# Optimization experiments

Measured on AMD Instinct MI355X. Metric: run time of the kernel, lower is better.

The kernel has to match this reference:

```python
import jax, jax.numpy as jnp
import numpy as np

N_STATES = 256
N_FEATURES = 32000
SEQ_LEN = 8192


def setup_inputs() -> dict:
    key = jax.random.key(0)
    k1, k2, k3, k4 = jax.random.split(key, 4)
    startprob = jax.random.uniform(k1, (N_STATES,), dtype=jnp.float32)
    startprob = startprob / startprob.sum()
    transmat = jax.random.uniform(k2, (N_STATES, N_STATES), dtype=jnp.float32)
    transmat = transmat / transmat.sum(axis=1, keepdims=True)
    emissionprob = jax.random.uniform(k3, (N_STATES, N_FEATURES), dtype=jnp.float32)
    emissionprob = emissionprob / emissionprob.sum(axis=1, keepdims=True)
    obs = jax.random.randint(k4, (SEQ_LEN,), 0, N_FEATURES, dtype=jnp.int64)
    return {"startprob": startprob, "transmat": transmat,
            "emissionprob": emissionprob, "obs": obs}


def reference(startprob, transmat, emissionprob, obs):
    """HMM forward algorithm (order-1, log-space).

    Returns alpha of shape (n_states, T) where
    alpha[i, t] = log P(O_1..O_t, q_t = S_i | theta).
    """
    log_start = jnp.log(startprob)                # [N]
    log_A = jnp.log(transmat)                     # [N, N]
    log_E = jnp.log(emissionprob)                 # [N, V]
    log_e_obs = log_E[:, obs].T                   # [T, N] gathered emissions

    alpha0 = log_start + log_e_obs[0]             # [N]

    def step(prev, log_e_t):
        # logsumexp over source state i: prev[i] + log_A[i, j]
        a = jax.nn.logsumexp(prev[:, None] + log_A, axis=0) + log_e_t
        return a, a

    _, alphas = jax.lax.scan(step, alpha0, log_e_obs[1:])   # [T-1, N]
    alpha = jnp.concatenate([alpha0[None, :], alphas], axis=0)  # [T, N]
    return alpha.T                                 # [N, T]
```

## Files before the change

kernel.cpp:

```cpp
#include <hip/hip_runtime.h>
#include <hip/hip_bf16.h>
#include <math.h>

#define NS 256
#define T_LEN 8192
#define NF 32000
#define L_CH 2
#define B_BN 8
#define S_TOT 10
#define C_CH 4096
#define G_CH 16
#define NBLK 256
#define SCALE 32768.0f
#define XPAD 264
#define TCHUNK 512

typedef short short8 __attribute__((ext_vector_type(8)));
typedef float f32x4 __attribute__((ext_vector_type(4)));

__device__ __forceinline__ short f2bs(float f) {
    union { __bf16 b; short s; } u; u.b = (__bf16)f; return u.s;
}
__device__ __forceinline__ float bs2f(short s) {
    union { short s; __bf16 b; } u; u.s = s; return (float)u.b;
}

__device__ __forceinline__ void sync_lds_only() {
    __builtin_amdgcn_sched_barrier(0);
    asm volatile("s_waitcnt lgkmcnt(0)" ::: "memory");
    __builtin_amdgcn_s_barrier();
    __builtin_amdgcn_sched_barrier(0);
}

__global__ __launch_bounds__(256)
void prep(const float* __restrict__ E, const int* __restrict__ obs,
          const float* __restrict__ A,
          unsigned short* __restrict__ SEb, short* __restrict__ Aswz) {
    const int bid = blockIdx.x;
    if (bid < 256) {
        const int jg = bid & 15, tc = bid >> 4;
        const int t0 = tc * TCHUNK;
        __shared__ int olds[TCHUNK];
        for (int i = threadIdx.x; i < TCHUNK; i += 256)
            olds[i] = obs[t0 + i];
        __syncthreads();
        const int jl = threadIdx.x & 15;
        const int tl = threadIdx.x >> 4;
        const int j  = jg * 16 + jl;
        const float* Erow = E + (size_t)j * NF;
#pragma unroll 4
        for (int p = 0; p < TCHUNK / 16; ++p) {
            int t_loc = p * 16 + tl;
            int o = olds[t_loc];
            SEb[(size_t)(t0 + t_loc) * NS + j] =
                (unsigned short)f2bs(Erow[o] * SCALE);
        }
    } else if (bid < 288) {
        const int pb   = (bid - 256) * 4 + (threadIdx.x >> 6);
        const int lane = threadIdx.x & 63;
        const int ntg  = pb >> 3;
        const int kk   = pb & 7;
        const int col  = ntg * 16 + (lane & 15);
        const int krow = kk * 32 + (lane >> 4) * 8;
        short8 v;
#pragma unroll
        for (int e = 0; e < 8; ++e)
            v[e] = f2bs(A[(size_t)(krow + e) * NS + col]);
        *(short8*)&Aswz[((size_t)pb * 64 + lane) * 8] = v;
    }
}

__global__ __launch_bounds__(1024, 4)
void hmm_chains(const float* __restrict__ start,
                const unsigned short* __restrict__ SEb,
                const short* __restrict__ Aswz,
                unsigned short* __restrict__ zbuf,
                float* __restrict__ Pb, float* __restrict__ Qb)
{
    const int bid  = blockIdx.x;
    const int tid  = threadIdx.x;
    const int wv   = tid >> 6;
    const int lane = tid & 63;
    const int cj   = lane & 15;
    const int rq   = lane >> 4;
    const int col  = wv * 16 + cj;
    const int base = 32 * bid - B_BN;

    __shared__ unsigned short xb[2][G_CH][XPAD];

    short8 bfr[8];
    const short8* Av = (const short8*)Aswz;
#pragma unroll
    for (int kk = 0; kk < 8; ++kk)
        bfr[kk] = Av[((size_t)(wv * 8 + kk)) * 64 + lane];
#pragma unroll
    for (int kk = 0; kk < 8; ++kk)
        asm volatile("" : "+v"(bfr[kk]));

    for (int idx = tid; idx < G_CH * XPAD; idx += 1024)
        ((unsigned short*)xb[0])[idx] = 0x3F80;

    float evc[4], evn[4];
#pragma unroll
    for (int r = 0; r < 4; ++r) {
        int t = base + 2 * (rq * 4 + r) + 1;
        t = t < 0 ? 0 : t;
        evc[r] = bs2f((short)SEb[(size_t)t * NS + col]);
    }

    for (int s = 1; s < S_TOT; ++s) {
        sync_lds_only();
        const int rb = (s - 1) & 1, wb = s & 1;

        if (s == B_BN && tid < 256) {
            int g = tid >> 4, part = tid & 15;
            float ss = 0.f;
            const unsigned short* row = &xb[rb][g][part * 16];
#pragma unroll
            for (int i = 0; i < 16; ++i) ss += bs2f(row[i]);
#pragma unroll
            for (int m = 1; m < 16; m <<= 1) ss += __shfl_xor(ss, m, 16);
            if (part == 0) Qb[bid * G_CH + g] = log2f(ss);
        }

#pragma unroll
        for (int r = 0; r < 4; ++r) {
            int t = base + 2 * (rq * 4 + r) + s + 1;
            t = t < 0 ? 0 : (t > T_LEN - 1 ? T_LEN - 1 : t);
            evn[r] = bs2f((short)SEb[(size_t)t * NS + col]);
        }

        short8 ax[8];
#pragma unroll
        for (int kk = 0; kk < 8; ++kk)
            ax[kk] = *(const short8*)&xb[rb][cj][kk * 32 + rq * 8];

        f32x4 acc = (f32x4){0.f, 0.f, 0.f, 0.f};
#pragma unroll
        for (int kk = 0; kk < 8; ++kk)
            acc = __builtin_amdgcn_mfma_f32_16x16x32_bf16(ax[kk], bfr[kk], acc, 0, 0, 0);

        const bool body = (s >= B_BN);
#pragma unroll
        for (int r = 0; r < 4; ++r) {
            int g = rq * 4 + r;
            float y = acc[r] * evc[r];
            bool skip = (bid == 0) && (s == B_BN) && (g == 0);
            if (!skip) {
                unsigned short yb = (unsigned short)f2bs(y);
                xb[wb][g][col] = yb;
                if (body) {
                    int tg = base + 2 * g + s;
                    zbuf[(size_t)tg * NS + col] = yb;
                }
            }
        }

        if (bid == 0 && s == B_BN && tid < 256) {
            float y0 = start[tid] * bs2f((short)SEb[tid]);
            unsigned short yb = (unsigned short)f2bs(y0);
            xb[wb][0][tid] = yb;
            zbuf[tid] = yb;
        }

#pragma unroll
        for (int r = 0; r < 4; ++r) evc[r] = evn[r];
    }

    sync_lds_only();
    if (tid < 256) {
        int g = tid >> 4, part = tid & 15;
        float ss = 0.f;
        const unsigned short* row = &xb[1][g][part * 16];
#pragma unroll
        for (int i = 0; i < 16; ++i) ss += bs2f(row[i]);
#pragma unroll
        for (int m = 1; m < 16; m <<= 1) ss += __shfl_xor(ss, m, 16);
        if (part == 0) Pb[bid * G_CH + g] = log2f(ss);
    }
}

__global__ __launch_bounds__(1024)
void hmm_stitch(const float* __restrict__ Pb,
                const float* __restrict__ Qb,
                float* __restrict__ Dfull)
{
    __shared__ double xs[1024];
    const int tid = threadIdx.x;
    double loc[4];
    double s = 0.0;
#pragma unroll
    for (int i = 0; i < 4; ++i) {
        int cc = tid * 4 + i;
        double d = (cc == 0) ? 0.0 : ((double)Pb[cc - 1] - (double)Qb[cc]);
        s += d;
        loc[i] = s;
    }
    xs[tid] = s;
    __syncthreads();
    for (int ofs = 1; ofs < 1024; ofs <<= 1) {
        double v = (tid >= ofs) ? xs[tid - ofs] : 0.0;
        __syncthreads();
        xs[tid] += v;
        __syncthreads();
    }
    const double off = xs[tid] - s;
#pragma unroll
    for (int i = 0; i < 4; ++i) {
        double D = off + loc[i];
        int t0 = (tid * 4 + i) * 2;
        Dfull[t0]     = (float)(D - 15.0 * (double)(t0 + 1));
        Dfull[t0 + 1] = (float)(D - 15.0 * (double)(t0 + 2));
    }
}

__global__ __launch_bounds__(256)
void hmm_finalize(const unsigned short* __restrict__ zbuf,
                  const float* __restrict__ Dfull,
                  float* __restrict__ out)
{
    __shared__ float tile[64][65];
    const int t0   = blockIdx.x * 64;
    const int j0   = blockIdx.y * 64;
    const int lane = threadIdx.x & 63;
    const int row4 = threadIdx.x >> 6;
    const float LN2 = 0.69314718055994530942f;

#pragma unroll
    for (int r = 0; r < 16; ++r) {
        int trow = r * 4 + row4;
        int t = t0 + trow;
        float z = bs2f((short)zbuf[(size_t)t * NS + j0 + lane]);
        tile[trow][lane] = __log2f(z) + Dfull[t];
    }
    __syncthreads();
#pragma unroll
    for (int r = 0; r < 16; ++r) {
        int jrow = r * 4 + row4;
        out[(size_t)(j0 + jrow) * T_LEN + t0 + lane] = LN2 * tile[lane][jrow];
    }
}

__global__ __launch_bounds__(NS, 1)
void hmm_forward_seq(const float* __restrict__ start,
                     const float* __restrict__ A,
                     const float* __restrict__ E,
                     const int* __restrict__ obs,
                     float* __restrict__ out)
{
    __shared__ float xbuf[2][NS];
    __shared__ float red[4];
    const int j = threadIdx.x;
    float a[NS];
#pragma unroll
    for (int i = 0; i < NS; ++i) a[i] = A[i * NS + j];
    const float LN2 = 0.69314718055994530942f;
    float Eacc = 0.0f;
    float z = start[j] * E[(size_t)j * NF + obs[0]] * SCALE;
    out[(size_t)j * T_LEN + 0] = LN2 * (__log2f(z) - 15.0f);
    xbuf[0][j] = z;
    __syncthreads();
    float se_cur = E[(size_t)j * NF + obs[1]] * SCALE;
    for (int t = 1; t < T_LEN; ++t) {
        float se_nxt = 0.0f;
        if (t + 1 < T_LEN) se_nxt = E[(size_t)j * NF + obs[t + 1]] * SCALE;
        const float4* x4 = (const float4*)xbuf[(t - 1) & 1];
        float y0 = 0.f, y1 = 0.f, y2 = 0.f, y3 = 0.f;
#pragma unroll
        for (int i = 0; i < NS / 4; ++i) {
            float4 xv = x4[i];
            y0 = fmaf(xv.x, a[4 * i + 0], y0);
            y1 = fmaf(xv.y, a[4 * i + 1], y1);
            y2 = fmaf(xv.z, a[4 * i + 2], y2);
            y3 = fmaf(xv.w, a[4 * i + 3], y3);
        }
        float y = ((y0 + y1) + (y2 + y3)) * se_cur;
        se_cur = se_nxt;
        out[(size_t)j * T_LEN + t] =
            LN2 * (__log2f(y) + Eacc - 15.0f * (float)(t + 1));
        float* wr = xbuf[t & 1];
        wr[j] = y;
        __syncthreads();
        if ((t & 1023) == 1023) {
            float v = wr[j];
#pragma unroll
            for (int d = 1; d < 64; d <<= 1) v = fmaxf(v, __shfl_xor(v, d, 64));
            if ((j & 63) == 0) red[j >> 6] = v;
            __syncthreads();
            float m = fmaxf(fmaxf(red[0], red[1]), fmaxf(red[2], red[3]));
            int k = ilogbf(m);
            wr[j] = ldexpf(wr[j], -k);
            Eacc += (float)k;
            __syncthreads();
        }
    }
}

extern "C" void kernel_launch(void* const* d_in, const int* in_sizes, int n_in,
                              void* d_out, int out_size, void* d_ws, size_t ws_size,
                              hipStream_t stream) {
    const float* start = (const float*)d_in[0];
    const float* A     = (const float*)d_in[1];
    const float* E     = (const float*)d_in[2];
    const int*   obs   = (const int*)d_in[3];
    float* out = (float*)d_out;

    char* ws = (char*)d_ws;
    const size_t zb_bytes  = (size_t)T_LEN * NS * sizeof(unsigned short);
    const size_t se_bytes  = (size_t)T_LEN * NS * sizeof(unsigned short);
    const size_t asw_bytes = (size_t)128 * 64 * 8 * sizeof(short);

    unsigned short* z   = (unsigned short*)ws;
    unsigned short* SEb = (unsigned short*)(ws + zb_bytes);
    short* Aswz  = (short*)(ws + zb_bytes + se_bytes);
    float* Pb    = (float*)(ws + zb_bytes + se_bytes + asw_bytes);
    float* Qb    = Pb + C_CH;
    float* Dfull = Qb + C_CH;

    const size_t need = zb_bytes + se_bytes + asw_bytes +
                        (2 * C_CH + T_LEN) * sizeof(float);

    if (ws_size >= need) {
        prep<<<288, 256, 0, stream>>>(E, obs, A, SEb, Aswz);
        hmm_chains<<<NBLK, 1024, 0, stream>>>(start, SEb, Aswz, z, Pb, Qb);
        hmm_stitch<<<1, 1024, 0, stream>>>(Pb, Qb, Dfull);
        hmm_finalize<<<dim3(T_LEN / 64, NS / 64), 256, 0, stream>>>(z, Dfull, out);
    } else {
        hmm_forward_seq<<<1, NS, 0, stream>>>(start, A, E, obs, out);
    }
}
```

Before: 37.95 us.

## Fuse stitch prefix-scan into finalize and use nontemporal stores

Removes the single-block hmm_stitch launch by having every finalize block redundantly compute the 4096-entry prefix scan of chunk offsets into shared memory. Finalize now runs 128 blocks that each loop over all four 64-state column tiles instead of using a 2D grid. Stores of intermediate and output buffers become nontemporal to reduce cache pollution. The trade-off is redundant scan work in each block, fewer blocks with more serial work, and a float rather than double subtraction of the per-step offset.

```diff
diff --git a/kernel.cpp b/kernel.cpp
--- a/kernel.cpp
+++ b/kernel.cpp
@@ -52,8 +52,8 @@
         for (int p = 0; p < TCHUNK / 16; ++p) {
             int t_loc = p * 16 + tl;
             int o = olds[t_loc];
-            SEb[(size_t)(t0 + t_loc) * NS + j] =
-                (unsigned short)f2bs(Erow[o] * SCALE);
+            unsigned short v = (unsigned short)f2bs(Erow[o] * SCALE);
+            __builtin_nontemporal_store(v, &SEb[(size_t)(t0 + t_loc) * NS + j]);
         }
     } else if (bid < 288) {
         const int pb   = (bid - 256) * 4 + (threadIdx.x >> 6);
@@ -151,7 +151,7 @@
                 xb[wb][g][col] = yb;
                 if (body) {
                     int tg = base + 2 * g + s;
-                    zbuf[(size_t)tg * NS + col] = yb;
+                    __builtin_nontemporal_store(yb, &zbuf[(size_t)tg * NS + col]);
                 }
             }
         }
@@ -160,7 +160,7 @@
             float y0 = start[tid] * bs2f((short)SEb[tid]);
             unsigned short yb = (unsigned short)f2bs(y0);
             xb[wb][0][tid] = yb;
-            zbuf[tid] = yb;
+            __builtin_nontemporal_store(yb, &zbuf[tid]);
         }
 
 #pragma unroll
@@ -180,25 +180,29 @@
     }
 }
 
-__global__ __launch_bounds__(1024)
-void hmm_stitch(const float* __restrict__ Pb,
-                const float* __restrict__ Qb,
-                float* __restrict__ Dfull)
+__global__ __launch_bounds__(256)
+void hmm_finalize(const unsigned short* __restrict__ zbuf,
+                  const float* __restrict__ Pb,
+                  const float* __restrict__ Qb,
+                  float* __restrict__ out)
 {
-    __shared__ double xs[1024];
+    __shared__ float Dd[C_CH];
+    __shared__ double xs[256];
+    __shared__ float tile[64][65];
     const int tid = threadIdx.x;
-    double loc[4];
+
+    double loc[16];
     double s = 0.0;
 #pragma unroll
-    for (int i = 0; i < 4; ++i) {
-        int cc = tid * 4 + i;
+    for (int i = 0; i < 16; ++i) {
+        int cc = tid * 16 + i;
         double d = (cc == 0) ? 0.0 : ((double)Pb[cc - 1] - (double)Qb[cc]);
         s += d;
         loc[i] = s;
     }
     xs[tid] = s;
     __syncthreads();
-    for (int ofs = 1; ofs < 1024; ofs <<= 1) {
+    for (int ofs = 1; ofs < 256; ofs <<= 1) {
         double v = (tid >= ofs) ? xs[tid - ofs] : 0.0;
         __syncthreads();
         xs[tid] += v;
@@ -206,38 +210,31 @@
     }
     const double off = xs[tid] - s;
 #pragma unroll
-    for (int i = 0; i < 4; ++i) {
-        double D = off + loc[i];
-        int t0 = (tid * 4 + i) * 2;
-        Dfull[t0]     = (float)(D - 15.0 * (double)(t0 + 1));
-        Dfull[t0 + 1] = (float)(D - 15.0 * (double)(t0 + 2));
-    }
-}
-
-__global__ __launch_bounds__(256)
-void hmm_finalize(const unsigned short* __restrict__ zbuf,
-                  const float* __restrict__ Dfull,
-                  float* __restrict__ out)
-{
-    __shared__ float tile[64][65];
+    for (int i = 0; i < 16; ++i)
+        Dd[tid * 16 + i] = (float)(off + loc[i]);
+    __syncthreads();
+
     const int t0   = blockIdx.x * 64;
-    const int j0   = blockIdx.y * 64;
-    const int lane = threadIdx.x & 63;
-    const int row4 = threadIdx.x >> 6;
+    const int lane = tid & 63;
+    const int row4 = tid >> 6;
     const float LN2 = 0.69314718055994530942f;
 
-#pragma unroll
-    for (int r = 0; r < 16; ++r) {
-        int trow = r * 4 + row4;
-        int t = t0 + trow;
-        float z = bs2f((short)zbuf[(size_t)t * NS + j0 + lane]);
-        tile[trow][lane] = __log2f(z) + Dfull[t];
-    }
-    __syncthreads();
-#pragma unroll
-    for (int r = 0; r < 16; ++r) {
-        int jrow = r * 4 + row4;
-        out[(size_t)(j0 + jrow) * T_LEN + t0 + lane] = LN2 * tile[lane][jrow];
+    for (int j0 = 0; j0 < NS; j0 += 64) {
+#pragma unroll
+        for (int r = 0; r < 16; ++r) {
+            int trow = r * 4 + row4;
+            int t = t0 + trow;
+            float z = bs2f((short)zbuf[(size_t)t * NS + j0 + lane]);
+            tile[trow][lane] = __log2f(z) + Dd[t >> 1] - 15.0f * (float)(t + 1);
+        }
+        __syncthreads();
+#pragma unroll
+        for (int r = 0; r < 16; ++r) {
+            int jrow = r * 4 + row4;
+            float v = LN2 * tile[lane][jrow];
+            __builtin_nontemporal_store(v, &out[(size_t)(j0 + jrow) * T_LEN + t0 + lane]);
+        }
+        __syncthreads();
     }
 }
 
@@ -312,19 +309,16 @@
 
     unsigned short* z   = (unsigned short*)ws;
     unsigned short* SEb = (unsigned short*)(ws + zb_bytes);
-    short* Aswz  = (short*)(ws + zb_bytes + se_bytes);
-    float* Pb    = (float*)(ws + zb_bytes + se_bytes + asw_bytes);
-    float* Qb    = Pb + C_CH;
-    float* Dfull = Qb + C_CH;
-
-    const size_t need = zb_bytes + se_bytes + asw_bytes +
-                        (2 * C_CH + T_LEN) * sizeof(float);
+    short* Aswz = (short*)(ws + zb_bytes + se_bytes);
+    float* Pb   = (float*)(ws + zb_bytes + se_bytes + asw_bytes);
+    float* Qb   = Pb + C_CH;
+
+    const size_t need = zb_bytes + se_bytes + asw_bytes + 2 * C_CH * sizeof(float);
 
     if (ws_size >= need) {
         prep<<<288, 256, 0, stream>>>(E, obs, A, SEb, Aswz);
         hmm_chains<<<NBLK, 1024, 0, stream>>>(start, SEb, Aswz, z, Pb, Qb);
-        hmm_stitch<<<1, 1024, 0, stream>>>(Pb, Qb, Dfull);
-        hmm_finalize<<<dim3(T_LEN / 64, NS / 64), 256, 0, stream>>>(z, Dfull, out);
+        hmm_finalize<<<T_LEN / 64, 256, 0, stream>>>(z, Pb, Qb, out);
     } else {
         hmm_forward_seq<<<1, NS, 0, stream>>>(start, A, E, obs, out);
     }
```

Measured after the change: 38.85 us. 1.02x slower.
